# Kernel tuning notes

Measured on AMD Instinct MI355X. Metric: run time of the kernel, lower is better.

## Reference

```python
import jax, jax.numpy as jnp
import numpy as np

N_EMBED = 1024
HEAD_SIZE = 64


def setup_inputs() -> dict:
    key = jax.random.key(0)
    kx, kk, kq, kv = jax.random.split(key, 4)
    B, T = 8, 2048
    x = jax.random.normal(kx, (B, T, N_EMBED), dtype=jnp.float32)
    # nn.Linear weights, stored as (in, out) so projection is x @ W
    s = 1.0 / np.sqrt(N_EMBED)
    Wk = jax.random.uniform(kk, (N_EMBED, HEAD_SIZE), jnp.float32, -s, s)
    Wq = jax.random.uniform(kq, (N_EMBED, HEAD_SIZE), jnp.float32, -s, s)
    Wv = jax.random.uniform(kv, (N_EMBED, HEAD_SIZE), jnp.float32, -s, s)
    return {"x": x, "Wk": Wk, "Wq": Wq, "Wv": Wv}


def reference(x, Wk, Wq, Wv):
    # x: [B, T, C] with C = n_embed
    C = x.shape[-1]
    k = x @ Wk  # [B, T, H]
    q = x @ Wq  # [B, T, H]
    v = x @ Wv  # [B, T, H]
    # NOTE: original scales by n_embed**-0.5, not head_size**-0.5
    wei = jnp.einsum("bth,bsh->bts", q, k) * (C ** -0.5)  # [B, T, T]
    wei = jax.nn.softmax(wei, axis=-1)
    # dropout = 0.0 (eval mode) -> identity
    out = jnp.einsum("bts,bsh->bth", wei, v)  # [B, T, H]
    return out
```

## Files before the change

kernel.cpp:

```cpp
#include <hip/hip_runtime.h>
#include <stdint.h>


#define B_ 8
#define T_ 2048
#define C_ 1024
#define H_ 64

typedef float f32x4 __attribute__((ext_vector_type(4)));
typedef short s16x8 __attribute__((ext_vector_type(8)));

__device__ __forceinline__ unsigned int rhu16(float f) {
    return (__float_as_uint(f) + 0x8000u) >> 16;
}
__device__ __forceinline__ unsigned int pkbf(float lo, float hi) {
    unsigned int a = __float_as_uint(lo) + 0x8000u;
    unsigned int b = __float_as_uint(hi) + 0x8000u;
    return __builtin_amdgcn_perm(b, a, 0x07060302u);
}
__device__ __forceinline__ void ld_lds16(const void* g, void* l) {
    __builtin_amdgcn_global_load_lds(
        (const __attribute__((address_space(1))) unsigned int*)g,
        (__attribute__((address_space(3))) unsigned int*)l, 16, 0, 0);
}

__global__ __launch_bounds__(256) void wconv(const float* __restrict__ Wk,
        const float* __restrict__ Wq, const float* __restrict__ Wv,
        unsigned short* __restrict__ Wt) {
    __shared__ float ls[64 * 65];
    const int bx = blockIdx.x, t = threadIdx.x;
    const int mat = bx >> 4, c0 = (bx & 15) << 6;
    const float* W = (mat == 0) ? Wk : ((mat == 1) ? Wq : Wv);
    const float sc = (mat == 1) ? 0.03125f : 1.0f;
    #pragma unroll
    for (int k = 0; k < 4; k++) {
        int i = t + (k << 8);
        int cr = i >> 4, hq = (i & 15) << 2;
        float4 v = *reinterpret_cast<const float4*>(&W[(size_t)(c0 + cr) * H_ + hq]);
        ls[cr * 65 + hq + 0] = v.x; ls[cr * 65 + hq + 1] = v.y;
        ls[cr * 65 + hq + 2] = v.z; ls[cr * 65 + hq + 3] = v.w;
    }
    __syncthreads();
    #pragma unroll
    for (int k = 0; k < 4; k++) {
        int i = t + (k << 8);
        int h = i >> 4, cq = (i & 15) << 2;
        float a = ls[(cq + 0) * 65 + h] * sc, b = ls[(cq + 1) * 65 + h] * sc;
        float c = ls[(cq + 2) * 65 + h] * sc, d = ls[(cq + 3) * 65 + h] * sc;
        uint2 o; o.x = pkbf(a, b); o.y = pkbf(c, d);
        *reinterpret_cast<uint2*>(&Wt[(size_t)(mat * 64 + h) * C_ + c0 + cq]) = o;
    }
}

__global__ __launch_bounds__(512) __attribute__((amdgpu_waves_per_eu(4, 4)))
void qkv(const float* __restrict__ x,
        const unsigned short* __restrict__ Wt,
        unsigned short* __restrict__ kb, unsigned short* __restrict__ qb,
        unsigned short* __restrict__ vtb) {
    __shared__ __align__(16) char smem[65536];
    char* xb = smem;
    char* wb = smem + 16384;

    const int t = threadIdx.x, lane = t & 63, w = t >> 6;
    const int l15 = lane & 15, quad = lane >> 4;
    const int bx = blockIdx.x;
    const int bb = bx >> 6;
    const int mt = bx & 63;
    const int m0 = bb * T_ + mt * 32;
    const int wr = w >> 2;
    const int colb = (w & 3) * 48;

    size_t xg; int xl;
    {
        int rg = w >> 2, j = w & 3;
        xg = (size_t)(m0 + rg * 16 + l15) * C_ + j * 16 + quad * 4;
        xl = w * 1024 + lane * 16;
    }
    size_t wg[3]; int wl[3];
    #pragma unroll
    for (int n = 0; n < 3; n++) {
        int g = w * 3 + n;
        wg[n] = (size_t)(g * 8 + (lane & 7)) * C_ + (lane >> 3) * 8;
        wl[n] = g * 1024 + lane * 16;
    }

    ld_lds16(x + xg, xb + xl);
    #pragma unroll
    for (int n = 0; n < 3; n++) ld_lds16(Wt + wg[n], wb + wl[n]);
    __syncthreads();

    f32x4 acc[3];
    #pragma unroll
    for (int ct = 0; ct < 3; ct++)
        #pragma unroll
        for (int j = 0; j < 4; j++) acc[ct][j] = 0.0f;

    #pragma unroll
    for (int i = 0; i < 16; i++) {
        const int cb = i & 1;
        const float* xc = (const float*)(xb + cb * 8192);
        const unsigned short* wcp = (const unsigned short*)(wb + cb * 24576);

        float4 xr[2][2];
        #pragma unroll
        for (int ks = 0; ks < 2; ks++)
            #pragma unroll
            for (int h = 0; h < 2; h++) {
                int c = ks * 32 + quad * 8 + h * 4;
                int j = c >> 4, u = (c & 15) >> 2;
                xr[ks][h] = *reinterpret_cast<const float4*>(
                    xc + (wr * 4 + j) * 256 + u * 64 + l15 * 4);
            }
        s16x8 wfr[3][2];
        #pragma unroll
        for (int ct = 0; ct < 3; ct++)
            #pragma unroll
            for (int ks = 0; ks < 2; ks++) {
                int col = colb + ct * 16 + l15;
                wfr[ct][ks] = *reinterpret_cast<const s16x8*>(
                    wcp + (col >> 3) * 512 + ((4 * ks + quad) * 8 + (col & 7)) * 8);
            }

        if (i < 15) {
            const int c1 = (i + 1) * 64;
            char* xn = xb + (cb ^ 1) * 8192;
            char* wn = wb + (cb ^ 1) * 24576;
            ld_lds16(x + xg + c1, xn + xl);
            #pragma unroll
            for (int n = 0; n < 3; n++) ld_lds16(Wt + wg[n] + c1, wn + wl[n]);
        }

        s16x8 af[2];
        #pragma unroll
        for (int ks = 0; ks < 2; ks++) {
            const float4 a = xr[ks][0], b = xr[ks][1];
            uint4 pk;
            pk.x = pkbf(a.x, a.y); pk.y = pkbf(a.z, a.w);
            pk.z = pkbf(b.x, b.y); pk.w = pkbf(b.z, b.w);
            af[ks] = *reinterpret_cast<s16x8*>(&pk);
        }
        #pragma unroll
        for (int ks = 0; ks < 2; ks++)
            #pragma unroll
            for (int ct = 0; ct < 3; ct++)
                acc[ct] = __builtin_amdgcn_mfma_f32_16x16x32_bf16(
                    af[ks], wfr[ct][ks], acc[ct], 0, 0, 0);
        __syncthreads();
    }

    #pragma unroll
    for (int ct = 0; ct < 3; ct++) {
        int cbv = colb + ct * 16;
        int sel = cbv >> 6;
        int h = (cbv & 63) + l15;
        int row0 = m0 + wr * 16 + quad * 4;
        if (sel < 2) {
            unsigned short* dst = sel ? qb : kb;
            #pragma unroll
            for (int r = 0; r < 4; r++)
                dst[(size_t)(row0 + r) * H_ + h] = (unsigned short)rhu16(acc[ct][r]);
        } else {
            int tt = row0 - bb * T_;
            uint2 pk;
            pk.x = pkbf(acc[ct][0], acc[ct][1]);
            pk.y = pkbf(acc[ct][2], acc[ct][3]);
            *reinterpret_cast<uint2*>(&vtb[((size_t)bb * H_ + h) * T_ + tt]) = pk;
        }
    }
}

__global__ __launch_bounds__(256, 2) void attn(
        const unsigned short* __restrict__ qb,
        const unsigned short* __restrict__ kb,
        const unsigned short* __restrict__ vtb,
        float* __restrict__ out) {
    __shared__ __align__(16) char smem[25728];

    const int t = threadIdx.x, lane = t & 63, w = t >> 6;
    const int l15 = lane & 15, quad = lane >> 4;
    const int bb = blockIdx.x & 7;
    const int q0 = (blockIdx.x >> 3) << 5;
    const size_t kbase = (size_t)bb * T_ * H_;
    unsigned short* Pw = (unsigned short*)(smem + w * 4608);

    s16x8 qf[2][2];
    #pragma unroll
    for (int rt = 0; rt < 2; rt++)
        #pragma unroll
        for (int ks = 0; ks < 2; ks++)
            qf[rt][ks] = *reinterpret_cast<const s16x8*>(
                &qb[kbase + (size_t)(q0 + rt * 16 + l15) * H_ + ks * 32 + quad * 8]);

    const int sw = w << 9;
    const unsigned short* kq = kb + kbase + (size_t)(sw + l15) * H_ + quad * 8;
    const unsigned short* vq[4];
    #pragma unroll
    for (int ht = 0; ht < 4; ht++)
        vq[ht] = vtb + ((size_t)bb * H_ + ht * 16 + l15) * T_ + sw + quad * 8;

    f32x4 oacc[2][4];
    #pragma unroll
    for (int rt = 0; rt < 2; rt++)
        #pragma unroll
        for (int ht = 0; ht < 4; ht++)
            #pragma unroll
            for (int j = 0; j < 4; j++) oacc[rt][ht][j] = 0.0f;
    float l_run[2] = {0.0f, 0.0f};
    const f32x4 z4 = {0.0f, 0.0f, 0.0f, 0.0f};

    for (int it = 0; it < 8; it++) {
        s16x8 kf[4][2], vf[2][4];
        #pragma unroll
        for (int st = 0; st < 4; st++)
            #pragma unroll
            for (int ks = 0; ks < 2; ks++)
                kf[st][ks] = *reinterpret_cast<const s16x8*>(
                    kq + (size_t)(it * 64 + st * 16) * H_ + ks * 32);
        #pragma unroll
        for (int ks2 = 0; ks2 < 2; ks2++)
            #pragma unroll
            for (int ht = 0; ht < 4; ht++)
                vf[ks2][ht] = *reinterpret_cast<const s16x8*>(
                    vq[ht] + it * 64 + ks2 * 32);

        f32x4 sacc[2][4];
        #pragma unroll
        for (int rt = 0; rt < 2; rt++)
            #pragma unroll
            for (int st = 0; st < 4; st++) {
                f32x4 s0v = __builtin_amdgcn_mfma_f32_16x16x32_bf16(
                    kf[st][0], qf[rt][0], z4, 0, 0, 0);
                sacc[rt][st] = __builtin_amdgcn_mfma_f32_16x16x32_bf16(
                    kf[st][1], qf[rt][1], s0v, 0, 0, 0);
            }

        #pragma unroll
        for (int rt = 0; rt < 2; rt++) {
            float ls = 0.0f;
            #pragma unroll
            for (int st = 0; st < 4; st++) {
                float p0 = __expf(sacc[rt][st][0]);
                float p1 = __expf(sacc[rt][st][1]);
                float p2 = __expf(sacc[rt][st][2]);
                float p3 = __expf(sacc[rt][st][3]);
                ls += (p0 + p1) + (p2 + p3);
                uint2 pk; pk.x = pkbf(p0, p1); pk.y = pkbf(p2, p3);
                *reinterpret_cast<uint2*>(
                    &Pw[(rt * 16 + l15) * 72 + st * 16 + quad * 4]) = pk;
            }
            l_run[rt] += ls;
        }

        #pragma unroll
        for (int rt = 0; rt < 2; rt++)
            #pragma unroll
            for (int ks2 = 0; ks2 < 2; ks2++) {
                s16x8 pf = *reinterpret_cast<const s16x8*>(
                    &Pw[(rt * 16 + l15) * 72 + ks2 * 32 + quad * 8]);
                #pragma unroll
                for (int ht = 0; ht < 4; ht++)
                    oacc[rt][ht] = __builtin_amdgcn_mfma_f32_16x16x32_bf16(
                        pf, vf[ks2][ht], oacc[rt][ht], 0, 0, 0);
            }
    }

    #pragma unroll
    for (int rt = 0; rt < 2; rt++) {
        l_run[rt] += __shfl_xor(l_run[rt], 16);
        l_run[rt] += __shfl_xor(l_run[rt], 32);
    }

    __syncthreads();
    float* Osf = (float*)smem;
    float* Ls  = (float*)smem + 3 * 32 * 66;
    if (w > 0) {
        int wi = w - 1;
        #pragma unroll
        for (int rt = 0; rt < 2; rt++) {
            if (quad == 0) Ls[wi * 32 + rt * 16 + l15] = l_run[rt];
            #pragma unroll
            for (int ht = 0; ht < 4; ht++)
                #pragma unroll
                for (int r = 0; r < 4; r++)
                    Osf[wi * 2112 + (rt * 16 + quad * 4 + r) * 66 + ht * 16 + l15] = oacc[rt][ht][r];
        }
    }
    __syncthreads();
    if (w == 0) {
        #pragma unroll
        for (int rt = 0; rt < 2; rt++)
            #pragma unroll
            for (int r = 0; r < 4; r++) {
                int row = rt * 16 + quad * 4 + r;
                float lt = __shfl(l_run[rt], quad * 4 + r)
                         + Ls[0 * 32 + row] + Ls[1 * 32 + row] + Ls[2 * 32 + row];
                float inv = 1.0f / lt;
                #pragma unroll
                for (int ht = 0; ht < 4; ht++) {
                    float o = oacc[rt][ht][r]
                            + Osf[0 * 2112 + row * 66 + ht * 16 + l15]
                            + Osf[1 * 2112 + row * 66 + ht * 16 + l15]
                            + Osf[2 * 2112 + row * 66 + ht * 16 + l15];
                    out[kbase + (size_t)(q0 + row) * H_ + ht * 16 + l15] = o * inv;
                }
            }
    }
}

extern "C" void kernel_launch(void* const* d_in, const int* in_sizes, int n_in,
                              void* d_out, int out_size, void* d_ws, size_t ws_size,
                              hipStream_t stream) {
    const float* x  = (const float*)d_in[0];
    const float* Wk = (const float*)d_in[1];
    const float* Wq = (const float*)d_in[2];
    const float* Wv = (const float*)d_in[3];

    unsigned short* kb  = (unsigned short*)d_ws;
    unsigned short* qbf = kb  + (size_t)B_ * T_ * H_;
    unsigned short* vtb = qbf + (size_t)B_ * T_ * H_;
    unsigned short* Wt  = (unsigned short*)d_out;

    wconv<<<48,  256, 0, stream>>>(Wk, Wq, Wv, Wt);
    qkv  <<<512, 512, 0, stream>>>(x, Wt, kb, qbf, vtb);
    attn <<<512, 256, 0, stream>>>(qbf, kb, vtb, (float*)d_out);
}
```

Measured before the change: 152.0 us.

## Deepen QKV projection LDS pipeline to four stages with counted vmcnt waits

Replaces the double-buffered LDS pipeline in the QKV projection kernel with a four-slot ring that has three chunks in flight. Each iteration waits with explicit s_waitcnt vmcnt counts and a single raw barrier, in place of two __syncthreads. The aim is to hide more global-load latency behind the MFMA work. In exchange it uses 128KB of LDS and relaxes the waves-per-EU hint, which reduces occupancy to one block per CU.

Result: slower. 164.2 us (+8.0%).

```diff
diff --git a/kernel.cpp b/kernel.cpp
--- a/kernel.cpp
+++ b/kernel.cpp
@@ -52,15 +52,12 @@
     }
 }
 
-__global__ __launch_bounds__(512) __attribute__((amdgpu_waves_per_eu(4, 4)))
+__global__ __launch_bounds__(512) __attribute__((amdgpu_waves_per_eu(2)))
 void qkv(const float* __restrict__ x,
         const unsigned short* __restrict__ Wt,
         unsigned short* __restrict__ kb, unsigned short* __restrict__ qb,
         unsigned short* __restrict__ vtb) {
-    __shared__ __align__(16) char smem[65536];
-    char* xb = smem;
-    char* wb = smem + 16384;
-
+    __shared__ __align__(16) char smem[131072];
     const int t = threadIdx.x, lane = t & 63, w = t >> 6;
     const int l15 = lane & 15, quad = lane >> 4;
     const int bx = blockIdx.x;
@@ -81,13 +78,17 @@
     for (int n = 0; n < 3; n++) {
         int g = w * 3 + n;
         wg[n] = (size_t)(g * 8 + (lane & 7)) * C_ + (lane >> 3) * 8;
-        wl[n] = g * 1024 + lane * 16;
-    }
-
-    ld_lds16(x + xg, xb + xl);
-    #pragma unroll
-    for (int n = 0; n < 3; n++) ld_lds16(Wt + wg[n], wb + wl[n]);
-    __syncthreads();
+        wl[n] = 8192 + g * 1024 + lane * 16;
+    }
+
+    #pragma unroll
+    for (int c = 0; c < 3; c++) {
+        char* cb = smem + c * 32768;
+        const int k0 = c * 64;
+        ld_lds16(x + xg + k0, cb + xl);
+        #pragma unroll
+        for (int n = 0; n < 3; n++) ld_lds16(Wt + wg[n] + k0, cb + wl[n]);
+    }
 
     f32x4 acc[3];
     #pragma unroll
@@ -97,9 +98,24 @@
 
     #pragma unroll
     for (int i = 0; i < 16; i++) {
-        const int cb = i & 1;
-        const float* xc = (const float*)(xb + cb * 8192);
-        const unsigned short* wcp = (const unsigned short*)(wb + cb * 24576);
+        if (i < 14)       asm volatile("s_waitcnt vmcnt(8)" ::: "memory");
+        else if (i == 14) asm volatile("s_waitcnt vmcnt(4)" ::: "memory");
+        else              asm volatile("s_waitcnt vmcnt(0)" ::: "memory");
+        __builtin_amdgcn_sched_barrier(0);
+        __builtin_amdgcn_s_barrier();
+        __builtin_amdgcn_sched_barrier(0);
+
+        if (i < 13) {
+            const int k3 = (i + 3) * 64;
+            char* nxt = smem + ((i + 3) & 3) * 32768;
+            ld_lds16(x + xg + k3, nxt + xl);
+            #pragma unroll
+            for (int n = 0; n < 3; n++) ld_lds16(Wt + wg[n] + k3, nxt + wl[n]);
+        }
+
+        const char* cur = smem + (i & 3) * 32768;
+        const float* xc = (const float*)cur;
+        const unsigned short* wcp = (const unsigned short*)(cur + 8192);
 
         float4 xr[2][2];
         #pragma unroll
@@ -120,15 +136,6 @@
                 wfr[ct][ks] = *reinterpret_cast<const s16x8*>(
                     wcp + (col >> 3) * 512 + ((4 * ks + quad) * 8 + (col & 7)) * 8);
             }
-
-        if (i < 15) {
-            const int c1 = (i + 1) * 64;
-            char* xn = xb + (cb ^ 1) * 8192;
-            char* wn = wb + (cb ^ 1) * 24576;
-            ld_lds16(x + xg + c1, xn + xl);
-            #pragma unroll
-            for (int n = 0; n < 3; n++) ld_lds16(Wt + wg[n] + c1, wn + wl[n]);
-        }
 
         s16x8 af[2];
         #pragma unroll
@@ -145,7 +152,6 @@
             for (int ct = 0; ct < 3; ct++)
                 acc[ct] = __builtin_amdgcn_mfma_f32_16x16x32_bf16(
                     af[ks], wfr[ct][ks], acc[ct], 0, 0, 0);
-        __syncthreads();
     }
 
     #pragma unroll
```

## Enlarge attention tile to 64 queries with 8 key-split waves per block

Applied to the files above, without the earlier changes.

The attention kernel now processes 64 query rows per block with 8 waves, each covering 256 keys, instead of 32 rows with 4 waves over 512 keys. Each K/V fragment loaded from global memory is reused across four query row tiles rather than two, which cuts K/V traffic per query. The cross-wave reduction now has all 8 waves write partial outputs to a large LDS buffer and then reduce rows in parallel, replacing the old scheme where wave 0 alone did the final sum. The cost is much larger LDS use per block (about 134 KB), higher register pressure from a doubled accumulator set, and half as many blocks in the grid.

New measurement: 142.6 us. 6.2% less time.

```diff
diff --git a/kernel.cpp b/kernel.cpp
--- a/kernel.cpp
+++ b/kernel.cpp
@@ -169,46 +169,47 @@
     }
 }
 
-__global__ __launch_bounds__(256, 2) void attn(
+__global__ __launch_bounds__(512) __attribute__((amdgpu_waves_per_eu(2, 2)))
+void attn(
         const unsigned short* __restrict__ qb,
         const unsigned short* __restrict__ kb,
         const unsigned short* __restrict__ vtb,
         float* __restrict__ out) {
-    __shared__ __align__(16) char smem[25728];
+    __shared__ __align__(16) char smem[137216];
 
     const int t = threadIdx.x, lane = t & 63, w = t >> 6;
     const int l15 = lane & 15, quad = lane >> 4;
     const int bb = blockIdx.x & 7;
-    const int q0 = (blockIdx.x >> 3) << 5;
+    const int q0 = (blockIdx.x >> 3) << 6;
     const size_t kbase = (size_t)bb * T_ * H_;
-    unsigned short* Pw = (unsigned short*)(smem + w * 4608);
-
-    s16x8 qf[2][2];
-    #pragma unroll
-    for (int rt = 0; rt < 2; rt++)
+    unsigned short* Pw = (unsigned short*)(smem + w * 9216);
+
+    s16x8 qf[4][2];
+    #pragma unroll
+    for (int rt = 0; rt < 4; rt++)
         #pragma unroll
         for (int ks = 0; ks < 2; ks++)
             qf[rt][ks] = *reinterpret_cast<const s16x8*>(
                 &qb[kbase + (size_t)(q0 + rt * 16 + l15) * H_ + ks * 32 + quad * 8]);
 
-    const int sw = w << 9;
+    const int sw = w << 8;
     const unsigned short* kq = kb + kbase + (size_t)(sw + l15) * H_ + quad * 8;
     const unsigned short* vq[4];
     #pragma unroll
     for (int ht = 0; ht < 4; ht++)
         vq[ht] = vtb + ((size_t)bb * H_ + ht * 16 + l15) * T_ + sw + quad * 8;
 
-    f32x4 oacc[2][4];
-    #pragma unroll
-    for (int rt = 0; rt < 2; rt++)
+    f32x4 oacc[4][4];
+    #pragma unroll
+    for (int rt = 0; rt < 4; rt++)
         #pragma unroll
         for (int ht = 0; ht < 4; ht++)
             #pragma unroll
             for (int j = 0; j < 4; j++) oacc[rt][ht][j] = 0.0f;
-    float l_run[2] = {0.0f, 0.0f};
+    float l_run[4] = {0.0f, 0.0f, 0.0f, 0.0f};
     const f32x4 z4 = {0.0f, 0.0f, 0.0f, 0.0f};
 
-    for (int it = 0; it < 8; it++) {
+    for (int it = 0; it < 4; it++) {
         s16x8 kf[4][2], vf[2][4];
         #pragma unroll
         for (int st = 0; st < 4; st++)
@@ -223,26 +224,23 @@
                 vf[ks2][ht] = *reinterpret_cast<const s16x8*>(
                     vq[ht] + it * 64 + ks2 * 32);
 
-        f32x4 sacc[2][4];
-        #pragma unroll
-        for (int rt = 0; rt < 2; rt++)
+        #pragma unroll
+        for (int rt = 0; rt < 4; rt++) {
+            f32x4 sacc[4];
             #pragma unroll
             for (int st = 0; st < 4; st++) {
                 f32x4 s0v = __builtin_amdgcn_mfma_f32_16x16x32_bf16(
                     kf[st][0], qf[rt][0], z4, 0, 0, 0);
-                sacc[rt][st] = __builtin_amdgcn_mfma_f32_16x16x32_bf16(
+                sacc[st] = __builtin_amdgcn_mfma_f32_16x16x32_bf16(
                     kf[st][1], qf[rt][1], s0v, 0, 0, 0);
             }
-
-        #pragma unroll
-        for (int rt = 0; rt < 2; rt++) {
             float ls = 0.0f;
             #pragma unroll
             for (int st = 0; st < 4; st++) {
-                float p0 = __expf(sacc[rt][st][0]);
-                float p1 = __expf(sacc[rt][st][1]);
-                float p2 = __expf(sacc[rt][st][2]);
-                float p3 = __expf(sacc[rt][st][3]);
+                float p0 = __expf(sacc[st][0]);
+                float p1 = __expf(sacc[st][1]);
+                float p2 = __expf(sacc[st][2]);
+                float p3 = __expf(sacc[st][3]);
                 ls += (p0 + p1) + (p2 + p3);
                 uint2 pk; pk.x = pkbf(p0, p1); pk.y = pkbf(p2, p3);
                 *reinterpret_cast<uint2*>(
@@ -252,7 +250,7 @@
         }
 
         #pragma unroll
-        for (int rt = 0; rt < 2; rt++)
+        for (int rt = 0; rt < 4; rt++)
             #pragma unroll
             for (int ks2 = 0; ks2 < 2; ks2++) {
                 s16x8 pf = *reinterpret_cast<const s16x8*>(
@@ -265,45 +263,35 @@
     }
 
     #pragma unroll
-    for (int rt = 0; rt < 2; rt++) {
+    for (int rt = 0; rt < 4; rt++) {
         l_run[rt] += __shfl_xor(l_run[rt], 16);
         l_run[rt] += __shfl_xor(l_run[rt], 32);
     }
 
     __syncthreads();
     float* Osf = (float*)smem;
-    float* Ls  = (float*)smem + 3 * 32 * 66;
-    if (w > 0) {
-        int wi = w - 1;
-        #pragma unroll
-        for (int rt = 0; rt < 2; rt++) {
-            if (quad == 0) Ls[wi * 32 + rt * 16 + l15] = l_run[rt];
-            #pragma unroll
-            for (int ht = 0; ht < 4; ht++)
-                #pragma unroll
-                for (int r = 0; r < 4; r++)
-                    Osf[wi * 2112 + (rt * 16 + quad * 4 + r) * 66 + ht * 16 + l15] = oacc[rt][ht][r];
-        }
+    float* Ls  = (float*)smem + 8 * 64 * 66;
+    #pragma unroll
+    for (int rt = 0; rt < 4; rt++) {
+        if (quad == 0) Ls[w * 64 + rt * 16 + l15] = l_run[rt];
+        #pragma unroll
+        for (int ht = 0; ht < 4; ht++)
+            #pragma unroll
+            for (int r = 0; r < 4; r++)
+                Osf[(w * 64 + rt * 16 + quad * 4 + r) * 66 + ht * 16 + l15]
+                    = oacc[rt][ht][r];
     }
     __syncthreads();
-    if (w == 0) {
-        #pragma unroll
-        for (int rt = 0; rt < 2; rt++)
-            #pragma unroll
-            for (int r = 0; r < 4; r++) {
-                int row = rt * 16 + quad * 4 + r;
-                float lt = __shfl(l_run[rt], quad * 4 + r)
-                         + Ls[0 * 32 + row] + Ls[1 * 32 + row] + Ls[2 * 32 + row];
-                float inv = 1.0f / lt;
-                #pragma unroll
-                for (int ht = 0; ht < 4; ht++) {
-                    float o = oacc[rt][ht][r]
-                            + Osf[0 * 2112 + row * 66 + ht * 16 + l15]
-                            + Osf[1 * 2112 + row * 66 + ht * 16 + l15]
-                            + Osf[2 * 2112 + row * 66 + ht * 16 + l15];
-                    out[kbase + (size_t)(q0 + row) * H_ + ht * 16 + l15] = o * inv;
-                }
-            }
+    #pragma unroll
+    for (int rr = 0; rr < 8; rr++) {
+        int row = w * 8 + rr;
+        float lt = 0.0f, o = 0.0f;
+        #pragma unroll
+        for (int wv = 0; wv < 8; wv++) {
+            lt += Ls[wv * 64 + row];
+            o  += Osf[(wv * 64 + row) * 66 + lane];
+        }
+        out[kbase + (size_t)(q0 + row) * H_ + lane] = o * (1.0f / lt);
     }
 }
 
@@ -322,5 +310,5 @@
 
     wconv<<<48,  256, 0, stream>>>(Wk, Wq, Wv, Wt);
     qkv  <<<512, 512, 0, stream>>>(x, Wt, kb, qbf, vtb);
-    attn <<<512, 256, 0, stream>>>(qbf, kb, vtb, (float*)d_out);
-}
+    attn <<<256, 512, 0, stream>>>(qbf, kb, vtb, (float*)d_out);
+}
```
